# Kernel optimization log

Hardware: AMD Instinct MI355X
Metric: run time of the kernel (lower is better)

The kernel has to match this reference:

```python
import jax, jax.numpy as jnp
import numpy as np

N_NODES = 100000
N_EDGES = 1600000
D_NODE = 96
D_EDGE = 32
N_GRAPHS = 128
BN_EPS = 1e-5


def setup_inputs() -> dict:
    key = jax.random.key(0)
    ks = jax.random.split(key, 8)
    x = jax.random.normal(ks[0], (N_NODES, D_NODE), dtype=jnp.float32)
    edge_attr = jax.random.normal(ks[1], (N_EDGES, D_EDGE), dtype=jnp.float32)
    edge_index = jax.random.randint(ks[2], (2, N_EDGES), 0, N_NODES, dtype=jnp.int64)
    batch = jnp.sort(jax.random.randint(ks[3], (N_NODES,), 0, N_GRAPHS, dtype=jnp.int64))
    W1 = jax.random.normal(ks[4], (16, D_NODE + D_EDGE), dtype=jnp.float32) * 0.09
    b1 = jax.random.normal(ks[5], (16,), dtype=jnp.float32) * 0.01
    gamma = jnp.ones((16,), dtype=jnp.float32)
    beta = jnp.zeros((16,), dtype=jnp.float32)
    run_mean = jnp.zeros((16,), dtype=jnp.float32)
    run_var = jnp.ones((16,), dtype=jnp.float32)
    W2 = jax.random.normal(ks[6], (1, 16), dtype=jnp.float32) * 0.25
    b2 = jax.random.normal(ks[7], (1,), dtype=jnp.float32) * 0.01
    return {"x": x, "edge_attr": edge_attr, "edge_index": edge_index, "batch": batch,
            "W1": W1, "b1": b1, "gamma": gamma, "beta": beta,
            "run_mean": run_mean, "run_var": run_var, "W2": W2, "b2": b2}


def reference(x, edge_attr, edge_index, batch, W1, b1, gamma, beta, run_mean, run_var, W2, b2):
    src, dst = edge_index[0], edge_index[1]
    # per-edge message: MLP(cat([x_j, edge_attr]))  -- [E, d_node+d_edge]
    msg_in = jnp.concatenate([x[src], edge_attr], axis=1)
    h = msg_in @ W1.T + b1                                  # [E, 16]
    # BatchNorm1d in eval mode (running stats); Dropout is identity in eval
    h = gamma * (h - run_mean) * jax.lax.rsqrt(run_var + BN_EPS) + beta
    h = jax.nn.relu(h)
    msg = h @ W2.T + b2                                     # [E, 1]
    # scatter-add messages to target nodes
    node_out = jax.ops.segment_sum(msg, dst, num_segments=N_NODES)   # [N, 1]
    # global add pool per graph
    pooled = jax.ops.segment_sum(node_out, batch, num_segments=N_GRAPHS)  # [G, 1]
    # mean over feature dim (size 1)
    return jnp.mean(pooled, axis=1)                         # [G]
```

## Files before the change

kernel.cpp:

```cpp
#include <hip/hip_runtime.h>

#define N_NODES 100000
#define N_EDGES 1600000
#define D_NODE 96
#define D_EDGE 32
#define N_GRAPHS 128
#define BN_EPS 1e-5f

#define EDGE_BLOCKS 6250
#define EDGE_THREADS 256
#define PT_STRIDE 6272

__global__ void prep_kernel(const float* __restrict__ W1, const float* __restrict__ b1,
                            const float* __restrict__ gamma, const float* __restrict__ beta,
                            const float* __restrict__ rmean, const float* __restrict__ rvar,
                            const float* __restrict__ W2, const float* __restrict__ b2,
                            float* __restrict__ w1n, float* __restrict__ w1e,
                            float* __restrict__ cw) {
    int t = threadIdx.x;
    if (t < 16) {
        float A = gamma[t] * rsqrtf(rvar[t] + BN_EPS);
        cw[t] = A * (b1[t] - rmean[t]) + beta[t];
        cw[16 + t] = W2[t];
        for (int j = 0; j < D_NODE; ++j)
            w1n[t * D_NODE + j] = A * W1[t * (D_NODE + D_EDGE) + j];
        for (int j = 0; j < D_EDGE; ++j)
            w1e[t * D_EDGE + j] = A * W1[t * (D_NODE + D_EDGE) + D_NODE + j];
    }
    if (t == 16) cw[32] = b2[0];
}

__global__ __launch_bounds__(256) void node_proj_kernel(const float* __restrict__ x,
                                                        const float* __restrict__ w1n,
                                                        float* __restrict__ y) {
    int t = threadIdx.x;
    int q = t >> 6;
    int n = blockIdx.x * 64 + (t & 63);
    if (n >= N_NODES) return;
    const float4* xr = (const float4*)(x + (size_t)n * D_NODE);
    const float* wq = w1n + (q * 4) * D_NODE;
    float acc[4];
#pragma unroll
    for (int kk = 0; kk < 4; ++kk) acc[kk] = 0.f;
#pragma unroll
    for (int j4 = 0; j4 < D_NODE / 4; ++j4) {
        float4 xv = xr[j4];
#pragma unroll
        for (int kk = 0; kk < 4; ++kk) {
            const float* w = wq + kk * D_NODE + j4 * 4;
            acc[kk] += xv.x * w[0] + xv.y * w[1] + xv.z * w[2] + xv.w * w[3];
        }
    }
    ((float4*)(y + (size_t)n * 16))[q] = make_float4(acc[0], acc[1], acc[2], acc[3]);
}

__global__ __launch_bounds__(EDGE_THREADS, 8) void edge_kernel(
    const float* __restrict__ ea, const int* __restrict__ eidx,
    const int* __restrict__ batch, const float* __restrict__ y,
    const float* __restrict__ w1e, const float* __restrict__ cw,
    float* __restrict__ partialsT) {
    __shared__ float bins[N_GRAPHS];
    int t = threadIdx.x;
    if (t < N_GRAPHS) bins[t] = 0.f;
    __syncthreads();

    int e = blockIdx.x * EDGE_THREADS + t;
    if (e < N_EDGES) {
        int s = eidx[e];
        int d = eidx[N_EDGES + e];
        int g = batch[d];

        float ya[16];
        const float4* yr = (const float4*)(y + (size_t)s * 16);
#pragma unroll
        for (int qq = 0; qq < 4; ++qq) ((float4*)ya)[qq] = yr[qq];

        const float4* er = (const float4*)(ea + (size_t)e * D_EDGE);
        float acc[16];
#pragma unroll
        for (int k = 0; k < 16; ++k) acc[k] = 0.f;
#pragma unroll 2
        for (int i = 0; i < 8; ++i) {
            float4 ev = er[i];
#pragma unroll
            for (int k = 0; k < 16; ++k) {
                const float* w = w1e + k * D_EDGE + i * 4;
                acc[k] += ev.x * w[0] + ev.y * w[1] + ev.z * w[2] + ev.w * w[3];
            }
        }

        float msg = cw[32];
#pragma unroll
        for (int k = 0; k < 16; ++k) {
            float h = acc[k] + ya[k] + cw[k];
            msg += fmaxf(h, 0.f) * cw[16 + k];
        }
        atomicAdd(&bins[g], msg);
    }

    __syncthreads();
    if (t < N_GRAPHS) partialsT[(size_t)t * PT_STRIDE + blockIdx.x] = bins[t];
}

__global__ __launch_bounds__(256) void reduce_kernel(const float* __restrict__ partialsT,
                                                     float* __restrict__ out) {
    __shared__ float sm[256];
    int g = blockIdx.x;
    float acc = 0.f;
    for (int b = threadIdx.x; b < EDGE_BLOCKS; b += 256)
        acc += partialsT[(size_t)g * PT_STRIDE + b];
    sm[threadIdx.x] = acc;
    __syncthreads();
    for (int w = 128; w > 0; w >>= 1) {
        if (threadIdx.x < w) sm[threadIdx.x] += sm[threadIdx.x + w];
        __syncthreads();
    }
    if (threadIdx.x == 0) out[g] = sm[0];
}

extern "C" void kernel_launch(void* const* d_in, const int* in_sizes, int n_in,
                              void* d_out, int out_size, void* d_ws, size_t ws_size,
                              hipStream_t stream) {
    const float* x     = (const float*)d_in[0];
    const float* ea    = (const float*)d_in[1];
    const int*   eidx  = (const int*)d_in[2];
    const int*   batch = (const int*)d_in[3];
    const float* W1    = (const float*)d_in[4];
    const float* b1    = (const float*)d_in[5];
    const float* gamma = (const float*)d_in[6];
    const float* beta  = (const float*)d_in[7];
    const float* rmean = (const float*)d_in[8];
    const float* rvar  = (const float*)d_in[9];
    const float* W2    = (const float*)d_in[10];
    const float* b2    = (const float*)d_in[11];
    float* out = (float*)d_out;

    float* ws = (float*)d_ws;
    float* w1n       = ws;
    float* w1e       = ws + 1536;
    float* cw        = ws + 2048;
    float* y         = ws + 4096;
    float* partialsT = ws + 4096 + (size_t)N_NODES * 16;

    prep_kernel<<<1, 64, 0, stream>>>(W1, b1, gamma, beta, rmean, rvar, W2, b2, w1n, w1e, cw);
    node_proj_kernel<<<(N_NODES + 63) / 64, 256, 0, stream>>>(x, w1n, y);
    edge_kernel<<<EDGE_BLOCKS, EDGE_THREADS, 0, stream>>>(ea, eidx, batch, y, w1e, cw, partialsT);
    reduce_kernel<<<N_GRAPHS, 256, 0, stream>>>(partialsT, out);
}
```

Measured before the change: 434.1 us.

## Process two edges per thread with all loads issued up front

The edge kernel now handles two edges per thread, split by a grid-wide stride, with half as many blocks. All loads for both edges (indices, edge attributes, gathered node projections, graph ids) are issued before any math, to raise memory-level parallelism and hide gather latency. The occupancy hint is dropped from launch bounds, and the per-block partials layout changes from graph-major to block-major, which also alters the reduce kernel's access pattern. Register pressure roughly doubles, which may lower occupancy, and the reduce kernel's reads become strided.

Measured after the change: 413.9 us. -4.7%, faster.

```diff
diff --git a/kernel.cpp b/kernel.cpp
--- a/kernel.cpp
+++ b/kernel.cpp
@@ -7,9 +7,9 @@
 #define N_GRAPHS 128
 #define BN_EPS 1e-5f
 
-#define EDGE_BLOCKS 6250
+#define EDGE_BLOCKS 3125
 #define EDGE_THREADS 256
-#define PT_STRIDE 6272
+#define EDGE_STRIDE (EDGE_BLOCKS * EDGE_THREADS)
 
 __global__ void prep_kernel(const float* __restrict__ W1, const float* __restrict__ b1,
                             const float* __restrict__ gamma, const float* __restrict__ beta,
@@ -54,61 +54,100 @@
     ((float4*)(y + (size_t)n * 16))[q] = make_float4(acc[0], acc[1], acc[2], acc[3]);
 }
 
-__global__ __launch_bounds__(EDGE_THREADS, 8) void edge_kernel(
+__global__ __launch_bounds__(EDGE_THREADS) void edge_kernel(
     const float* __restrict__ ea, const int* __restrict__ eidx,
     const int* __restrict__ batch, const float* __restrict__ y,
     const float* __restrict__ w1e, const float* __restrict__ cw,
-    float* __restrict__ partialsT) {
+    float* __restrict__ partials) {
     __shared__ float bins[N_GRAPHS];
     int t = threadIdx.x;
     if (t < N_GRAPHS) bins[t] = 0.f;
     __syncthreads();
 
-    int e = blockIdx.x * EDGE_THREADS + t;
-    if (e < N_EDGES) {
-        int s = eidx[e];
-        int d = eidx[N_EDGES + e];
-        int g = batch[d];
+    int e0 = blockIdx.x * EDGE_THREADS + t;
+    int e1 = e0 + EDGE_STRIDE;
 
-        float ya[16];
-        const float4* yr = (const float4*)(y + (size_t)s * 16);
+    int s0 = eidx[e0];
+    int d0 = eidx[N_EDGES + e0];
+    int s1 = eidx[e1];
+    int d1 = eidx[N_EDGES + e1];
+
+    const float4* er0 = (const float4*)(ea + (size_t)e0 * D_EDGE);
+    const float4* er1 = (const float4*)(ea + (size_t)e1 * D_EDGE);
+    float4 eva[8], evb[8];
 #pragma unroll
-        for (int qq = 0; qq < 4; ++qq) ((float4*)ya)[qq] = yr[qq];
+    for (int i = 0; i < 8; ++i) eva[i] = er0[i];
+#pragma unroll
+    for (int i = 0; i < 8; ++i) evb[i] = er1[i];
 
-        const float4* er = (const float4*)(ea + (size_t)e * D_EDGE);
+    float ya0[16], ya1[16];
+    const float4* yr0 = (const float4*)(y + (size_t)s0 * 16);
+    const float4* yr1 = (const float4*)(y + (size_t)s1 * 16);
+#pragma unroll
+    for (int qq = 0; qq < 4; ++qq) ((float4*)ya0)[qq] = yr0[qq];
+#pragma unroll
+    for (int qq = 0; qq < 4; ++qq) ((float4*)ya1)[qq] = yr1[qq];
+
+    int g0 = batch[d0];
+    int g1 = batch[d1];
+
+    float b2v = cw[32];
+
+    {
         float acc[16];
 #pragma unroll
         for (int k = 0; k < 16; ++k) acc[k] = 0.f;
-#pragma unroll 2
+#pragma unroll
         for (int i = 0; i < 8; ++i) {
-            float4 ev = er[i];
+            float4 ev = eva[i];
 #pragma unroll
             for (int k = 0; k < 16; ++k) {
                 const float* w = w1e + k * D_EDGE + i * 4;
                 acc[k] += ev.x * w[0] + ev.y * w[1] + ev.z * w[2] + ev.w * w[3];
             }
         }
-
-        float msg = cw[32];
+        float msg = b2v;
 #pragma unroll
         for (int k = 0; k < 16; ++k) {
-            float h = acc[k] + ya[k] + cw[k];
+            float h = acc[k] + ya0[k] + cw[k];
             msg += fmaxf(h, 0.f) * cw[16 + k];
         }
-        atomicAdd(&bins[g], msg);
+        atomicAdd(&bins[g0], msg);
+    }
+
+    {
+        float acc[16];
+#pragma unroll
+        for (int k = 0; k < 16; ++k) acc[k] = 0.f;
+#pragma unroll
+        for (int i = 0; i < 8; ++i) {
+            float4 ev = evb[i];
+#pragma unroll
+            for (int k = 0; k < 16; ++k) {
+                const float* w = w1e + k * D_EDGE + i * 4;
+                acc[k] += ev.x * w[0] + ev.y * w[1] + ev.z * w[2] + ev.w * w[3];
+            }
+        }
+        float msg = b2v;
+#pragma unroll
+        for (int k = 0; k < 16; ++k) {
+            float h = acc[k] + ya1[k] + cw[k];
+            msg += fmaxf(h, 0.f) * cw[16 + k];
+        }
+        atomicAdd(&bins[g1], msg);
     }
 
     __syncthreads();
-    if (t < N_GRAPHS) partialsT[(size_t)t * PT_STRIDE + blockIdx.x] = bins[t];
+    if (t < N_GRAPHS) partials[(size_t)blockIdx.x * N_GRAPHS + t] = bins[t];
 }
 
-__global__ __launch_bounds__(256) void reduce_kernel(const float* __restrict__ partialsT,
+__global__ __launch_bounds__(256) void reduce_kernel(const float* __restrict__ partials,
                                                      float* __restrict__ out) {
     __shared__ float sm[256];
     int g = blockIdx.x;
     float acc = 0.f;
     for (int b = threadIdx.x; b < EDGE_BLOCKS; b += 256)
-        acc += partialsT[(size_t)g * PT_STRIDE + b];
+        acc += partials[(size_t)b * N_GRAPHS + g];
     sm[threadIdx.x] = acc;
     __syncthreads();
     for (int w = 128; w > 0; w >>= 1) {
@@ -136,14 +175,14 @@
     float* out = (float*)d_out;
 
     float* ws = (float*)d_ws;
-    float* w1n       = ws;
-    float* w1e       = ws + 1536;
-    float* cw        = ws + 2048;
-    float* y         = ws + 4096;
-    float* partialsT = ws + 4096 + (size_t)N_NODES * 16;
+    float* w1n      = ws;
+    float* w1e      = ws + 1536;
+    float* cw       = ws + 2048;
+    float* y        = ws + 4096;
+    float* partials = ws + 4096 + (size_t)N_NODES * 16;
 
     prep_kernel<<<1, 64, 0, stream>>>(W1, b1, gamma, beta, rmean, rvar, W2, b2, w1n, w1e, cw);
     node_proj_kernel<<<(N_NODES + 63) / 64, 256, 0, stream>>>(x, w1n, y);
-    edge_kernel<<<EDGE_BLOCKS, EDGE_THREADS, 0, stream>>>(ea, eidx, batch, y, w1e, cw, partialsT);
-    reduce_kernel<<<N_GRAPHS, 256, 0, stream>>>(partialsT, out);
+    edge_kernel<<<EDGE_BLOCKS, EDGE_THREADS, 0, stream>>>(ea, eidx, batch, y, w1e, cw, partials);
+    reduce_kernel<<<N_GRAPHS, 256, 0, stream>>>(partials, out);
 }
```
